# Optimization experiments

Hardware: AMD Instinct MI355X
Metric: run time of the kernel (lower is better)

## Reference

```python
import jax, jax.numpy as jnp
import numpy as np
import math

B, T, C, H, L, V = 4, 2048, 256, 4, 2, 1024
HS = C // H  # head size


def setup_inputs() -> dict:
    key = jax.random.key(0)
    ks = jax.random.split(key, 10)
    s = 0.02
    return {
        "tokens": jax.random.randint(ks[0], (B, T), 0, V),
        "wte": s * jax.random.normal(ks[1], (V + 1, C), dtype=jnp.float32),
        "ln1_g": jnp.ones((L, C), jnp.float32),
        "ln1_b": jnp.zeros((L, C), jnp.float32),
        "attn_w": s * jax.random.normal(ks[2], (L, 3 * C, C), dtype=jnp.float32),
        "attn_b": jnp.zeros((L, 3 * C), jnp.float32),
        "proj_w": s * jax.random.normal(ks[3], (L, C, C), dtype=jnp.float32),
        "proj_b": jnp.zeros((L, C), jnp.float32),
        "embk": s * jax.random.normal(ks[4], (L, T, HS), dtype=jnp.float32),
        "embv": s * jax.random.normal(ks[5], (L, T, HS), dtype=jnp.float32),
        "ln2_g": jnp.ones((L, C), jnp.float32),
        "ln2_b": jnp.zeros((L, C), jnp.float32),
        "fc_w": s * jax.random.normal(ks[6], (L, 4 * C, C), dtype=jnp.float32),
        "fc_b": jnp.zeros((L, 4 * C), jnp.float32),
        "mproj_w": s * jax.random.normal(ks[7], (L, C, 4 * C), dtype=jnp.float32),
        "mproj_b": jnp.zeros((L, C), jnp.float32),
        "lnf_g": jnp.ones((C,), jnp.float32),
        "lnf_b": jnp.zeros((C,), jnp.float32),
        "head_w": s * jax.random.normal(ks[8], (V, C), dtype=jnp.float32),
    }


def _ln(x, g, b):
    mu = x.mean(-1, keepdims=True)
    var = x.var(-1, keepdims=True)
    return (x - mu) / jnp.sqrt(var + 1e-5) * g + b


def _gelu(x):  # NewGELU (tanh approximation)
    return 0.5 * x * (1.0 + jnp.tanh(math.sqrt(2.0 / math.pi) * (x + 0.044715 * x ** 3)))


def reference(tokens, wte, ln1_g, ln1_b, attn_w, attn_b, proj_w, proj_b,
              embk, embv, ln2_g, ln2_b, fc_w, fc_b, mproj_w, mproj_b,
              lnf_g, lnf_b, head_w):
    x = wte[tokens]  # [B,T,C]; no absolute pos emb in this model
    idx = jnp.arange(T)
    rel = jnp.tril(idx[:, None] - idx[None, :])  # [T,T] nonneg offsets
    causal = idx[:, None] >= idx[None, :]
    scale = 1.0 / math.sqrt(HS)
    for l in range(L):
        h = _ln(x, ln1_g[l], ln1_b[l])
        qkv = h @ attn_w[l].T + attn_b[l]  # [B,T,3C]
        q, k, v = jnp.split(qkv, 3, axis=-1)
        q = q.reshape(B, T, H, HS).transpose(0, 2, 1, 3)  # [B,H,T,hs]
        k = k.reshape(B, T, H, HS).transpose(0, 2, 1, 3)
        v = v.reshape(B, T, H, HS).transpose(0, 2, 1, 3)
        rk = embk[l][rel]  # [T,T,hs]
        rv = embv[l][rel]  # [T,T,hs]
        att = jnp.einsum('bhtd,bhsd->bhts', q, k) * scale \
            + jnp.einsum('bhtd,tsd->bhts', q, rk)
        att = jnp.where(causal, att, -jnp.inf)
        att = jax.nn.softmax(att, axis=-1)
        y = jnp.einsum('bhts,bhsd->bhtd', att, v) \
            + jnp.einsum('bhts,tsd->bhtd', att, rv)
        y = y.transpose(0, 2, 1, 3).reshape(B, T, C)
        x = x + (y @ proj_w[l].T + proj_b[l])
        h2 = _ln(x, ln2_g[l], ln2_b[l])
        x = x + (_gelu(h2 @ fc_w[l].T + fc_b[l]) @ mproj_w[l].T + mproj_b[l])
    x = _ln(x, lnf_g, lnf_b)
    return x @ head_w.T  # [B,T,V] logits
```

## Files before the change

### kernel.cpp

```cpp
#include <hip/hip_runtime.h>
#include <hip/hip_bf16.h>
#include <math.h>

#define BB 4
#define TT 2048
#define CC 256
#define HH 4
#define LL 2
#define VV 1024
#define HS 64
#define EPAD 2176
#define LOG2E 1.4426950408889634f

typedef __attribute__((ext_vector_type(8))) __bf16 bf16x8;
typedef __attribute__((ext_vector_type(4))) float f32x4;

#define MFMA16(a, b, c) __builtin_amdgcn_mfma_f32_16x16x32_bf16((a), (b), (c), 0, 0, 0)

__device__ __forceinline__ ushort f2bf(float f) {
    __hip_bfloat16 h = __float2bfloat16(f);
    return *reinterpret_cast<ushort*>(&h);
}
__device__ __forceinline__ float bf2f(ushort u) {
    union { uint i; float f; } c; c.i = ((uint)u) << 16; return c.f;
}

__device__ __forceinline__ void gload16(const void* g, void* l) {
    __builtin_amdgcn_global_load_lds(
        (const __attribute__((address_space(1))) void*)g,
        (__attribute__((address_space(3))) void*)l, 16, 0, 0);
}

__device__ __forceinline__ float gelu_f(float v) {
    return 0.5f * v * (1.0f + tanhf(0.7978845608028654f * (v + 0.044715f * v * v * v)));
}

__global__ void embed_kernel(const int* __restrict__ tok,
                             const float* __restrict__ wte,
                             float* __restrict__ x) {
    int row = blockIdx.x;
    int tid = threadIdx.x;
    int tk = tok[row];
    x[(size_t)row * CC + tid] = wte[(size_t)tk * CC + tid];
}

__global__ void cvt5_kernel(const float* __restrict__ w0, const float* __restrict__ w1,
                            const float* __restrict__ w2, const float* __restrict__ w3,
                            const float* __restrict__ w4,
                            ushort* __restrict__ o0, ushort* __restrict__ o1,
                            ushort* __restrict__ o2, ushort* __restrict__ o3,
                            ushort* __restrict__ o4) {
    int i = blockIdx.x * 256 + threadIdx.x;
    const float* src; ushort* dst; int j;
    if (i < 98304)       { src = w0; dst = o0; j = i; }
    else if (i < 131072) { src = w1; dst = o1; j = i - 98304; }
    else if (i < 262144) { src = w2; dst = o2; j = i - 131072; }
    else if (i < 393216) { src = w3; dst = o3; j = i - 262144; }
    else                 { src = w4; dst = o4; j = i - 393216; }
    float4 v = ((const float4*)src)[j];
    ushort4 o;
    o.x = f2bf(v.x); o.y = f2bf(v.y); o.z = f2bf(v.z); o.w = f2bf(v.w);
    ((ushort4*)dst)[j] = o;
}

__global__ __launch_bounds__(256) void ln_kernel(const float* __restrict__ x,
                                                 const float* __restrict__ g,
                                                 const float* __restrict__ b,
                                                 ushort* __restrict__ out) {
    int row = blockIdx.x * 4 + (threadIdx.x >> 6);
    int lane = threadIdx.x & 63;
    float4 v = ((const float4*)(x + (size_t)row * CC))[lane];
    float s = v.x + v.y + v.z + v.w;
    float s2 = v.x * v.x + v.y * v.y + v.z * v.z + v.w * v.w;
    for (int m = 1; m < 64; m <<= 1) {
        s += __shfl_xor(s, m);
        s2 += __shfl_xor(s2, m);
    }
    float mean = s * (1.0f / CC);
    float var = s2 * (1.0f / CC) - mean * mean;
    float rs = rsqrtf(var + 1e-5f);
    float4 gg = ((const float4*)g)[lane];
    float4 bb = ((const float4*)b)[lane];
    ushort4 o;
    o.x = f2bf((v.x - mean) * rs * gg.x + bb.x);
    o.y = f2bf((v.y - mean) * rs * gg.y + bb.y);
    o.z = f2bf((v.z - mean) * rs * gg.z + bb.z);
    o.w = f2bf((v.w - mean) * rs * gg.w + bb.w);
    ((ushort4*)(out + (size_t)row * CC))[lane] = o;
}

template<int MODE>
__global__ __launch_bounds__(512) void bgemm256_kernel(
        const ushort* __restrict__ A, const ushort* __restrict__ W,
        const float* __restrict__ bias, float* __restrict__ out,
        ushort* __restrict__ outb, int N, int K,
        ushort* __restrict__ qb, ushort* __restrict__ kb,
        ushort* __restrict__ vtb) {
    constexpr int BUFSH = 16 * 512;
    __shared__ ushort lds[2 * BUFSH];
    int tid = threadIdx.x;
    int w = tid >> 6, lane = tid & 63;
    int lo = lane & 15, hi = lane >> 4;
    int row0 = blockIdx.y * 128;
    int col0 = blockIdx.x * 128;
    int wm = w >> 2, wn = w & 3;
    const ushort* Asrc = A + (size_t)row0 * K;
    const ushort* Wsrc = W + (size_t)col0 * K;

    auto STAGE = [&](int buf, int k0) {
        ushort* dst = &lds[buf * BUFSH];
        gload16(Asrc + (size_t)(w * 16 + lo) * K + k0 + hi * 8, dst + w * 512);
        gload16(Wsrc + (size_t)(w * 16 + lo) * K + k0 + hi * 8, dst + (8 + w) * 512);
    };

    f32x4 acc[4][2] = {};
    int NT = K >> 5;
    STAGE(0, 0);
    asm volatile("s_waitcnt vmcnt(0)" ::: "memory");
    __syncthreads();
    for (int t = 0; t < NT; ++t) {
        int buf = t & 1;
        if (t + 1 < NT) STAGE(buf ^ 1, (t + 1) << 5);
        bf16x8 a[4], b[2];
#pragma unroll
        for (int f = 0; f < 4; ++f)
            a[f] = *(const bf16x8*)&lds[buf * BUFSH + (wm * 4 + f) * 512 + lane * 8];
#pragma unroll
        for (int g = 0; g < 2; ++g)
            b[g] = *(const bf16x8*)&lds[buf * BUFSH + (8 + wn * 2 + g) * 512 + lane * 8];
        __builtin_amdgcn_s_setprio(1);
#pragma unroll
        for (int f = 0; f < 4; ++f)
#pragma unroll
            for (int g = 0; g < 2; ++g)
                acc[f][g] = MFMA16(a[f], b[g], acc[f][g]);
        __builtin_amdgcn_s_setprio(0);
        asm volatile("s_waitcnt vmcnt(0)" ::: "memory");
        __syncthreads();
    }
#pragma unroll
    for (int f = 0; f < 4; ++f) {
        int rr = row0 + wm * 64 + f * 16 + hi * 4;
#pragma unroll
        for (int g = 0; g < 2; ++g) {
            int cc = col0 + wn * 32 + g * 16 + lo;
            float bv = bias ? bias[cc] : 0.0f;
#pragma unroll
            for (int j = 0; j < 4; ++j) {
                int r = rr + j;
                float v = acc[f][g][j] + bv;
                if (MODE == 3) {
                    int t = r & 2047, bb2 = r >> 11;
                    int which = cc >> 8, hh = (cc >> 6) & 3, dd = cc & 63;
                    size_t bh = (size_t)(bb2 * 4 + hh);
                    if (which == 0)      qb[(bh * 2048 + t) * 64 + dd] = f2bf(v);
                    else if (which == 1) kb[(bh * 2048 + t) * 64 + dd] = f2bf(v * (0.125f * LOG2E));
                    else                 vtb[(bh * 64 + dd) * 2048 + t] = f2bf(v);
                } else if (MODE == 2) {
                    outb[(size_t)r * N + cc] = f2bf(gelu_f(v));
                } else {
                    out[(size_t)r * N + cc] = v;
                }
            }
        }
    }
}

__global__ __launch_bounds__(256) void bgemm64_kernel(
        const ushort* __restrict__ A, const ushort* __restrict__ W,
        const float* __restrict__ bias, float* __restrict__ out,
        int N, int K) {
    constexpr int ASUB = 8, TOT = 16, BUFSH = 128 * 64;
    __shared__ ushort lds[2 * BUFSH];
    int tid = threadIdx.x;
    int w = tid >> 6, lane = tid & 63;
    int lo = lane & 15, hi = lane >> 4;
    int row0 = blockIdx.y * 64;
    int col0 = blockIdx.x * 64;
    const ushort* Asrc = A + (size_t)row0 * K;
    const ushort* Wsrc = W + (size_t)col0 * K;

    auto STAGE = [&](int buf, int k0) {
        ushort* dst = &lds[buf * BUFSH];
        for (int s = w; s < TOT; s += 4) {
            const ushort* src;
            if (s < ASUB) {
                int rg = s >> 1, kh = s & 1;
                src = Asrc + (size_t)(rg * 16 + lo) * K + k0 + kh * 32 + hi * 8;
            } else {
                int s2 = s - ASUB;
                int cg = s2 >> 1, kh = s2 & 1;
                src = Wsrc + (size_t)(cg * 16 + lo) * K + k0 + kh * 32 + hi * 8;
            }
            gload16(src, dst + s * 512);
        }
    };

    f32x4 acc[4] = {};
    int NT = K >> 6;
    STAGE(0, 0);
    asm volatile("s_waitcnt vmcnt(0)" ::: "memory");
    __syncthreads();
    for (int t = 0; t < NT; ++t) {
        int buf = t & 1;
        if (t + 1 < NT) STAGE(buf ^ 1, (t + 1) << 6);
        bf16x8 a[2];
#pragma unroll
        for (int kh = 0; kh < 2; ++kh)
            a[kh] = *(const bf16x8*)&lds[buf * BUFSH + (w * 2 + kh) * 512 + lane * 8];
        __builtin_amdgcn_s_setprio(1);
#pragma unroll
        for (int g = 0; g < 4; ++g) {
#pragma unroll
            for (int kh = 0; kh < 2; ++kh) {
                bf16x8 b = *(const bf16x8*)&lds[buf * BUFSH + (ASUB + g * 2 + kh) * 512 + lane * 8];
                acc[g] = MFMA16(a[kh], b, acc[g]);
            }
        }
        __builtin_amdgcn_s_setprio(0);
        asm volatile("s_waitcnt vmcnt(0)" ::: "memory");
        __syncthreads();
    }
#pragma unroll
    for (int g = 0; g < 4; ++g) {
        int cc = col0 + g * 16 + lo;
        float bv = bias ? bias[cc] : 0.0f;
#pragma unroll
        for (int j = 0; j < 4; ++j) {
            int r = row0 + w * 16 + hi * 4 + j;
            out[(size_t)r * N + cc] += acc[g][j] + bv;
        }
    }
}

__global__ void emb_bf2_kernel(const float* __restrict__ ek,
                               const float* __restrict__ ev,
                               ushort* __restrict__ ekp,
                               ushort* __restrict__ evtp) {
    int i = blockIdx.x * 256 + threadIdx.x;
    int l = i / (EPAD * 64);
    int j = i - l * (EPAD * 64);
    int rp = j >> 6, d = j & 63;
    int o = rp - 64;
    bool in = (o >= 0 && o < TT);
    float kv = in ? ek[(size_t)l * TT * HS + (size_t)o * 64 + d] * LOG2E : 0.0f;
    float vv = in ? ev[(size_t)l * TT * HS + (size_t)o * 64 + d] : 0.0f;
    ekp[(size_t)l * EPAD * 64 + (size_t)rp * 64 + d] = f2bf(kv);
    evtp[(size_t)l * 64 * EPAD + (size_t)d * EPAD + rp] = f2bf(vv);
}

#define SBUF 57344
#define KOFF 0
#define VOFF 8192
#define EKOFF 16384
#define EVOFF 32768
#define WSCR (2 * SBUF)

__global__ __launch_bounds__(512, 2) void flash_kernel(
        const ushort* __restrict__ qb,
        const ushort* __restrict__ kb,
        const ushort* __restrict__ vtb,
        const ushort* __restrict__ ekp,
        const ushort* __restrict__ evtp,
        ushort* __restrict__ y) {
    extern __shared__ __align__(16) char dls[];

    int g = blockIdx.x;
    int lbid = ((g & 7) << 5) | (g >> 3);
    int bh = lbid >> 4;
    int pk = lbid & 15;
    int tid = threadIdx.x;
    int w = tid >> 6;
    int sub = w & 3;
    int h = w >> 2;
    int lane = tid & 63;
    int lo = lane & 15, hi = lane >> 4;
    int sw = (lo & 7) << 4;

    char* wbase = dls + WSCR + w * 6144;
    ushort (*Rl)[88]   = (ushort (*)[88])  wbase;
    ushort (*Pl)[72]   = (ushort (*)[72])  wbase;
    ushort (*Ppl)[104] = (ushort (*)[104])(wbase + 2816);

    {
        uint* pz = reinterpret_cast<uint*>(&Ppl[0][0]);
        for (int i = lane; i < 832; i += 64) pz[i] = 0;
    }

    const char* kB  = (const char*)(kb  + (size_t)bh * 2048 * 64);
    const char* vB  = (const char*)(vtb + (size_t)bh * 64 * 2048);
    const char* ekB = (const char*)ekp;
    const char* evB = (const char*)evtp;

    int t0A = (31 - pk) * 64, t0B = pk * 64;
    int NSA = 32 - pk;
    const int NC = 33;

    auto STAGE = [&](int buf, int ci) {
        int t0 = (ci < NSA) ? t0A : t0B;
        int s0 = ((ci < NSA) ? ci : ci - NSA) * 64;
        int band0 = t0 - s0;
        char* B = dls + buf * SBUF;
        int wb = (tid & 448) << 4;
        {
            int gb = tid * 16;
            int r = gb >> 7, c = gb & 127;
            gload16(kB + (size_t)(s0 + r) * 128 + (c ^ ((r & 7) << 4)), B + KOFF + wb);
        }
        {
            int gb = tid * 16;
            int r = gb >> 7, c = gb & 127;
            gload16(vB + (size_t)r * 4096 + (size_t)s0 * 2 + (c ^ ((r & 7) << 4)),
                    B + VOFF + wb);
        }
#pragma unroll
        for (int p = 0; p < 2; ++p) {
            int gb = p * 8192 + tid * 16;
            int r = gb >> 7, c = gb & 127;
            gload16(ekB + (size_t)(band0 + r) * 128 + (c ^ ((r & 7) << 4)),
                    B + EKOFF + p * 8192 + wb);
        }
#pragma unroll
        for (int p = 0; p < 3; ++p) {
            int gb = p * 8192 + tid * 16;
            int r = gb / 384, c = gb - r * 384;
            gload16(evB + (size_t)r * 4352 + (size_t)band0 * 2 + (c ^ ((r & 7) << 4)),
                    B + EVOFF + p * 8192 + wb);
        }
    };

    STAGE(0, 0);
    asm volatile("s_waitcnt vmcnt(0)" ::: "memory");
    __syncthreads();

    int b_ = bh >> 2, h_ = bh & 3;
    int buf = 0, ci = 0;
    int nb = h ? 0 : 2;
    int kcA = h ? 0 : 1, kcB = h ? 1 : 2;

    for (int tile = 0; tile < 2; ++tile) {
        int t0 = tile ? t0B : t0A;
        int NS = tile ? (pk + 1) : NSA;

        const ushort* qbase = qb + ((size_t)bh * 2048 + t0 + sub * 16) * 64;
        bf16x8 qf0 = *(const bf16x8*)(qbase + (size_t)lo * 64 + hi * 8);
        bf16x8 qf1 = *(const bf16x8*)(qbase + (size_t)lo * 64 + 32 + hi * 8);

        float rs[4] = {0.0f, 0.0f, 0.0f, 0.0f};
        f32x4 O[4] = {};

        for (int c = 0; c < NS; ++c, ++ci) {
            if (ci + 1 < NC) STAGE(buf ^ 1, ci + 1);
            const char* B = dls + buf * SBUF;
            bool diag = (c == NS - 1);

            f32x4 sacc[2] = {};
            __builtin_amdgcn_s_setprio(1);
#pragma unroll
            for (int ni = 0; ni < 2; ++ni) {
                int R = (2 * h + ni) * 16 + lo;
                bf16x8 b0 = *(const bf16x8*)(B + KOFF + R * 128 + ((hi * 16) ^ sw));
                bf16x8 b1 = *(const bf16x8*)(B + KOFF + R * 128 + ((64 + hi * 16) ^ sw));
                sacc[ni] = MFMA16(qf0, b0, sacc[ni]);
                sacc[ni] = MFMA16(qf1, b1, sacc[ni]);
            }
#pragma unroll
            for (int ni = 0; ni < 3; ++ni) {
                int n = nb + ni;
                int RL = (sub + n) * 16 + lo;
                f32x4 r = {};
                bf16x8 e0 = *(const bf16x8*)(B + EKOFF + RL * 128 + ((hi * 16) ^ sw));
                bf16x8 e1 = *(const bf16x8*)(B + EKOFF + RL * 128 + ((64 + hi * 16) ^ sw));
                r = MFMA16(qf0, e0, r);
                r = MFMA16(qf1, e1, r);
#pragma unroll
                for (int j = 0; j < 4; ++j) Rl[hi * 4 + j][n * 16 + lo] = f2bf(r[j]);
            }
            __builtin_amdgcn_s_setprio(0);
            float sv[2][4];
#pragma unroll
            for (int ni = 0; ni < 2; ++ni) {
                int sl = (2 * h + ni) * 16 + lo;
#pragma unroll
                for (int j = 0; j < 4; ++j) {
                    int r_ = hi * 4 + j;
                    sv[ni][j] = sacc[ni][j] + bf2f(Rl[r_][r_ - sl + 64]);
                }
            }
            asm volatile("" ::: "memory");
#pragma unroll
            for (int ni = 0; ni < 2; ++ni) {
                int sl = (2 * h + ni) * 16 + lo;
#pragma unroll
                for (int j = 0; j < 4; ++j) {
                    int r_ = hi * 4 + j;
                    float p = (!diag || sl <= sub * 16 + r_) ? exp2f(sv[ni][j]) : 0.0f;
                    rs[j] += p;
                    ushort pu = f2bf(p);
                    Pl[r_][sl] = pu;
                    Ppl[r_][r_ - sl + 64] = pu;
                }
            }
            asm volatile("" ::: "memory");

            __builtin_amdgcn_s_setprio(1);
            bf16x8 pa  = *(const bf16x8*)(&Pl[lo][h * 32 + hi * 8]);
            bf16x8 pb0 = *(const bf16x8*)(&Ppl[lo][kcA * 32 + hi * 8]);
            bf16x8 pb1 = *(const bf16x8*)(&Ppl[lo][kcB * 32 + hi * 8]);
#pragma unroll
            for (int n = 0; n < 4; ++n) {
                int R = n * 16 + lo;
                bf16x8 bv = *(const bf16x8*)(B + VOFF + R * 128 + ((h * 64 + hi * 16) ^ sw));
                O[n] = MFMA16(pa, bv, O[n]);
                bf16x8 e0 = *(const bf16x8*)(B + EVOFF + R * 384 +
                                             ((sub * 32 + kcA * 64 + hi * 16) ^ sw));
                O[n] = MFMA16(pb0, e0, O[n]);
                bf16x8 e1 = *(const bf16x8*)(B + EVOFF + R * 384 +
                                             ((sub * 32 + kcB * 64 + hi * 16) ^ sw));
                O[n] = MFMA16(pb1, e1, O[n]);
            }
            __builtin_amdgcn_s_setprio(0);
            asm volatile("" ::: "memory");

            asm volatile("s_waitcnt vmcnt(0)" ::: "memory");
            __syncthreads();
            buf ^= 1;
        }

#pragma unroll
        for (int msk = 1; msk < 16; msk <<= 1)
#pragma unroll
            for (int j = 0; j < 4; ++j) rs[j] += __shfl_xor(rs[j], msk);

        char* mscr = dls + (buf ^ 1) * SBUF + sub * 8192;
        if (h == 1) {
            float* Of = (float*)mscr;
#pragma unroll
            for (int n = 0; n < 4; ++n)
#pragma unroll
                for (int j = 0; j < 4; ++j)
                    Of[(hi * 4 + j) * 64 + n * 16 + lo] = O[n][j];
            if (lo == 0)
#pragma unroll
                for (int j = 0; j < 4; ++j)
                    ((float*)(mscr + 4096))[hi * 4 + j] = rs[j];
        }
        __syncthreads();
        if (h == 0) {
            float* Of = (float*)mscr;
            float inv[4];
#pragma unroll
            for (int j = 0; j < 4; ++j)
                inv[j] = 1.0f / (rs[j] + ((float*)(mscr + 4096))[hi * 4 + j]);
#pragma unroll
            for (int n = 0; n < 4; ++n)
#pragma unroll
                for (int j = 0; j < 4; ++j) {
                    int r = t0 + sub * 16 + hi * 4 + j;
                    float v = O[n][j] + Of[(hi * 4 + j) * 64 + n * 16 + lo];
                    y[((size_t)(b_ * 2048 + r)) * 256 + h_ * 64 + n * 16 + lo] =
                        f2bf(v * inv[j]);
                }
        }
        __syncthreads();
    }
}

extern "C" void kernel_launch(void* const* d_in, const int* in_sizes, int n_in,
                              void* d_out, int out_size, void* d_ws, size_t ws_size,
                              hipStream_t stream) {
    const int*   tokens  = (const int*)d_in[0];
    const float* wte     = (const float*)d_in[1];
    const float* ln1_g   = (const float*)d_in[2];
    const float* ln1_b   = (const float*)d_in[3];
    const float* attn_w  = (const float*)d_in[4];
    const float* attn_b  = (const float*)d_in[5];
    const float* proj_w  = (const float*)d_in[6];
    const float* proj_b  = (const float*)d_in[7];
    const float* embk    = (const float*)d_in[8];
    const float* embv    = (const float*)d_in[9];
    const float* ln2_g   = (const float*)d_in[10];
    const float* ln2_b   = (const float*)d_in[11];
    const float* fc_w    = (const float*)d_in[12];
    const float* fc_b    = (const float*)d_in[13];
    const float* mproj_w = (const float*)d_in[14];
    const float* mproj_b = (const float*)d_in[15];
    const float* lnf_g   = (const float*)d_in[16];
    const float* lnf_b   = (const float*)d_in[17];
    const float* head_w  = (const float*)d_in[18];
    float* out = (float*)d_out;

    const int M = BB * TT;
    char* wsb = (char*)d_ws;
    float*  x    = (float*)wsb;
    ushort* h    = (ushort*)(wsb + ((size_t)8 << 20));
    ushort* y    = (ushort*)(wsb + ((size_t)12 << 20));
    ushort* qb   = (ushort*)(wsb + ((size_t)16 << 20));
    ushort* kbf  = (ushort*)(wsb + ((size_t)20 << 20));
    ushort* vtb  = (ushort*)(wsb + ((size_t)24 << 20));
    ushort* ekp  = (ushort*)(wsb + ((size_t)28 << 20));
    ushort* evtp = ekp + (size_t)LL * EPAD * 64;
    ushort* attn_wb  = (ushort*)(wsb + ((size_t)30 << 20));
    ushort* proj_wb  = attn_wb + (size_t)LL * 3 * CC * CC;
    ushort* fc_wb    = proj_wb + (size_t)LL * CC * CC;
    ushort* mproj_wb = fc_wb + (size_t)LL * 4 * CC * CC;
    ushort* head_wb  = mproj_wb + (size_t)LL * CC * 4 * CC;
    ushort* fcb = (ushort*)d_out;

    dim3 blk(256);
    const int FLDS = WSCR + 8 * 6144;
    hipFuncSetAttribute(reinterpret_cast<const void*>(flash_kernel),
                        hipFuncAttributeMaxDynamicSharedMemorySize, FLDS);

    cvt5_kernel<<<dim3(1792), blk, 0, stream>>>(
        attn_w, proj_w, fc_w, mproj_w, head_w,
        attn_wb, proj_wb, fc_wb, mproj_wb, head_wb);
    emb_bf2_kernel<<<dim3(LL * EPAD * 64 / 256), blk, 0, stream>>>(
        embk, embv, ekp, evtp);
    embed_kernel<<<dim3(M), blk, 0, stream>>>(tokens, wte, x);

    for (int l = 0; l < LL; l++) {
        ln_kernel<<<dim3(M / 4), blk, 0, stream>>>(x, ln1_g + l * CC, ln1_b + l * CC, h);
        bgemm256_kernel<3><<<dim3(6, 64), dim3(512), 0, stream>>>(
            h, attn_wb + (size_t)l * 3 * CC * CC, attn_b + (size_t)l * 3 * CC,
            nullptr, nullptr, 3 * CC, CC, qb, kbf, vtb);
        flash_kernel<<<dim3(256), dim3(512), FLDS, stream>>>(
            qb, kbf, vtb, ekp + (size_t)l * EPAD * 64, evtp + (size_t)l * 64 * EPAD, y);
        bgemm64_kernel<<<dim3(4, 128), blk, 0, stream>>>(
            y, proj_wb + (size_t)l * CC * CC, proj_b + (size_t)l * CC,
            x, CC, CC);
        ln_kernel<<<dim3(M / 4), blk, 0, stream>>>(x, ln2_g + l * CC, ln2_b + l * CC, h);
        bgemm256_kernel<2><<<dim3(8, 64), dim3(512), 0, stream>>>(
            h, fc_wb + (size_t)l * 4 * CC * CC, fc_b + (size_t)l * 4 * CC,
            nullptr, fcb, 4 * CC, CC, nullptr, nullptr, nullptr);
        bgemm64_kernel<<<dim3(4, 128), blk, 0, stream>>>(
            fcb, mproj_wb + (size_t)l * CC * 4 * CC, mproj_b + (size_t)l * CC,
            x, CC, 4 * CC);
    }

    ln_kernel<<<dim3(M / 4), blk, 0, stream>>>(x, lnf_g, lnf_b, h);
    bgemm256_kernel<0><<<dim3(8, 64), dim3(512), 0, stream>>>(
        h, head_wb, nullptr, out, nullptr, VV, CC, nullptr, nullptr, nullptr);
}
```

Measured before the change: 331.0 us.

## Fuse residual-add and LayerNorm into projection GEMMs; merge prep and embed kernels

The two residual projection GEMMs (attn proj and MLP proj) now compute a full 256-wide row strip per block of 32 rows. Each block adds bias and residual, then reduces row statistics through shuffles and LDS to emit the next LayerNorm's bf16 output directly. This removes the separate ln kernels. The embedding lookup is fused with the first LayerNorm, and the weight and relative-embedding conversion kernels are merged into one launch. The cost is fewer, larger blocks: 256 blocks, each re-streaming the whole weight matrix, and the extra LDS may lower occupancy.

```diff
diff --git a/kernel.cpp b/kernel.cpp
--- a/kernel.cpp
+++ b/kernel.cpp
@@ -35,41 +35,49 @@
     return 0.5f * v * (1.0f + tanhf(0.7978845608028654f * (v + 0.044715f * v * v * v)));
 }
 
-__global__ void embed_kernel(const int* __restrict__ tok,
-                             const float* __restrict__ wte,
-                             float* __restrict__ x) {
-    int row = blockIdx.x;
-    int tid = threadIdx.x;
-    int tk = tok[row];
-    x[(size_t)row * CC + tid] = wte[(size_t)tk * CC + tid];
-}
-
-__global__ void cvt5_kernel(const float* __restrict__ w0, const float* __restrict__ w1,
+__global__ void prep_kernel(const float* __restrict__ w0, const float* __restrict__ w1,
                             const float* __restrict__ w2, const float* __restrict__ w3,
                             const float* __restrict__ w4,
                             ushort* __restrict__ o0, ushort* __restrict__ o1,
                             ushort* __restrict__ o2, ushort* __restrict__ o3,
-                            ushort* __restrict__ o4) {
-    int i = blockIdx.x * 256 + threadIdx.x;
-    const float* src; ushort* dst; int j;
-    if (i < 98304)       { src = w0; dst = o0; j = i; }
-    else if (i < 131072) { src = w1; dst = o1; j = i - 98304; }
-    else if (i < 262144) { src = w2; dst = o2; j = i - 131072; }
-    else if (i < 393216) { src = w3; dst = o3; j = i - 262144; }
-    else                 { src = w4; dst = o4; j = i - 393216; }
-    float4 v = ((const float4*)src)[j];
-    ushort4 o;
-    o.x = f2bf(v.x); o.y = f2bf(v.y); o.z = f2bf(v.z); o.w = f2bf(v.w);
-    ((ushort4*)dst)[j] = o;
-}
-
-__global__ __launch_bounds__(256) void ln_kernel(const float* __restrict__ x,
-                                                 const float* __restrict__ g,
-                                                 const float* __restrict__ b,
-                                                 ushort* __restrict__ out) {
+                            ushort* __restrict__ o4,
+                            const float* __restrict__ ek, const float* __restrict__ ev,
+                            ushort* __restrict__ ekp, ushort* __restrict__ evtp) {
+    int bi = blockIdx.x;
+    if (bi < 1792) {
+        int i = bi * 256 + threadIdx.x;
+        const float* src; ushort* dst; int j;
+        if (i < 98304)       { src = w0; dst = o0; j = i; }
+        else if (i < 131072) { src = w1; dst = o1; j = i - 98304; }
+        else if (i < 262144) { src = w2; dst = o2; j = i - 131072; }
+        else if (i < 393216) { src = w3; dst = o3; j = i - 262144; }
+        else                 { src = w4; dst = o4; j = i - 393216; }
+        float4 v = ((const float4*)src)[j];
+        ushort4 o;
+        o.x = f2bf(v.x); o.y = f2bf(v.y); o.z = f2bf(v.z); o.w = f2bf(v.w);
+        ((ushort4*)dst)[j] = o;
+    } else {
+        int i = (bi - 1792) * 256 + threadIdx.x;
+        int l = i / (EPAD * 64);
+        int j = i - l * (EPAD * 64);
+        int rp = j >> 6, d = j & 63;
+        int o = rp - 64;
+        bool in = (o >= 0 && o < TT);
+        float kv = in ? ek[(size_t)l * TT * HS + (size_t)o * 64 + d] * LOG2E : 0.0f;
+        float vv = in ? ev[(size_t)l * TT * HS + (size_t)o * 64 + d] : 0.0f;
+        ekp[(size_t)l * EPAD * 64 + (size_t)rp * 64 + d] = f2bf(kv);
+        evtp[(size_t)l * 64 * EPAD + (size_t)d * EPAD + rp] = f2bf(vv);
+    }
+}
+
+__global__ __launch_bounds__(256) void embed_ln_kernel(
+        const int* __restrict__ tok, const float* __restrict__ wte,
+        const float* __restrict__ g, const float* __restrict__ b,
+        float* __restrict__ x, ushort* __restrict__ h) {
     int row = blockIdx.x * 4 + (threadIdx.x >> 6);
     int lane = threadIdx.x & 63;
-    float4 v = ((const float4*)(x + (size_t)row * CC))[lane];
+    int tk = tok[row];
+    float4 v = ((const float4*)(wte + (size_t)tk * CC))[lane];
     float s = v.x + v.y + v.z + v.w;
     float s2 = v.x * v.x + v.y * v.y + v.z * v.z + v.w * v.w;
     for (int m = 1; m < 64; m <<= 1) {
@@ -86,7 +94,8 @@
     o.y = f2bf((v.y - mean) * rs * gg.y + bb.y);
     o.z = f2bf((v.z - mean) * rs * gg.z + bb.z);
     o.w = f2bf((v.w - mean) * rs * gg.w + bb.w);
-    ((ushort4*)(out + (size_t)row * CC))[lane] = o;
+    ((float4*)(x + (size_t)row * CC))[lane] = v;
+    ((ushort4*)(h + (size_t)row * CC))[lane] = o;
 }
 
 template<int MODE>
@@ -166,87 +175,112 @@
     }
 }
 
-__global__ __launch_bounds__(256) void bgemm64_kernel(
+template<int NSTEP>
+__global__ __launch_bounds__(512) void bgemmln_kernel(
         const ushort* __restrict__ A, const ushort* __restrict__ W,
-        const float* __restrict__ bias, float* __restrict__ out,
-        int N, int K) {
-    constexpr int ASUB = 8, TOT = 16, BUFSH = 128 * 64;
-    __shared__ ushort lds[2 * BUFSH];
+        const float* __restrict__ bias, float* __restrict__ x,
+        const float* __restrict__ lng, const float* __restrict__ lnb,
+        ushort* __restrict__ hout) {
+    extern __shared__ ushort plds[];
+    constexpr int K = NSTEP * 64;
+    constexpr int BUFSH = 36 * 512;
     int tid = threadIdx.x;
     int w = tid >> 6, lane = tid & 63;
     int lo = lane & 15, hi = lane >> 4;
-    int row0 = blockIdx.y * 64;
-    int col0 = blockIdx.x * 64;
+    int row0 = blockIdx.x * 32;
+    int wm = w >> 2, wn = w & 3;
     const ushort* Asrc = A + (size_t)row0 * K;
-    const ushort* Wsrc = W + (size_t)col0 * K;
 
     auto STAGE = [&](int buf, int k0) {
-        ushort* dst = &lds[buf * BUFSH];
-        for (int s = w; s < TOT; s += 4) {
+        ushort* dst = &plds[buf * BUFSH];
+        for (int s = w; s < 36; s += 8) {
             const ushort* src;
-            if (s < ASUB) {
+            if (s < 4) {
                 int rg = s >> 1, kh = s & 1;
                 src = Asrc + (size_t)(rg * 16 + lo) * K + k0 + kh * 32 + hi * 8;
             } else {
-                int s2 = s - ASUB;
-                int cg = s2 >> 1, kh = s2 & 1;
-                src = Wsrc + (size_t)(cg * 16 + lo) * K + k0 + kh * 32 + hi * 8;
+                int sb = s - 4, cg = sb >> 1, kh = sb & 1;
+                src = W + (size_t)(cg * 16 + lo) * K + k0 + kh * 32 + hi * 8;
             }
             gload16(src, dst + s * 512);
         }
     };
 
     f32x4 acc[4] = {};
-    int NT = K >> 6;
     STAGE(0, 0);
     asm volatile("s_waitcnt vmcnt(0)" ::: "memory");
     __syncthreads();
-    for (int t = 0; t < NT; ++t) {
+    for (int t = 0; t < NSTEP; ++t) {
         int buf = t & 1;
-        if (t + 1 < NT) STAGE(buf ^ 1, (t + 1) << 6);
+        if (t + 1 < NSTEP) STAGE(buf ^ 1, (t + 1) << 6);
         bf16x8 a[2];
 #pragma unroll
         for (int kh = 0; kh < 2; ++kh)
-            a[kh] = *(const bf16x8*)&lds[buf * BUFSH + (w * 2 + kh) * 512 + lane * 8];
+            a[kh] = *(const bf16x8*)&plds[buf * BUFSH + (wm * 2 + kh) * 512 + lane * 8];
         __builtin_amdgcn_s_setprio(1);
 #pragma unroll
-        for (int g = 0; g < 4; ++g) {
+        for (int g2 = 0; g2 < 4; ++g2) {
 #pragma unroll
             for (int kh = 0; kh < 2; ++kh) {
-                bf16x8 b = *(const bf16x8*)&lds[buf * BUFSH + (ASUB + g * 2 + kh) * 512 + lane * 8];
-                acc[g] = MFMA16(a[kh], b, acc[g]);
+                bf16x8 b = *(const bf16x8*)&plds[buf * BUFSH + 2048 +
+                                                 ((wn * 4 + g2) * 2 + kh) * 512 + lane * 8];
+                acc[g2] = MFMA16(a[kh], b, acc[g2]);
             }
         }
         __builtin_amdgcn_s_setprio(0);
         asm volatile("s_waitcnt vmcnt(0)" ::: "memory");
         __syncthreads();
     }
-#pragma unroll
-    for (int g = 0; g < 4; ++g) {
-        int cc = col0 + g * 16 + lo;
-        float bv = bias ? bias[cc] : 0.0f;
+
+    float* part = (float*)&plds[2 * BUFSH];
+    float v[4][4];
+    float s1[4] = {0, 0, 0, 0}, s2[4] = {0, 0, 0, 0};
+#pragma unroll
+    for (int g2 = 0; g2 < 4; ++g2) {
+        int cc = wn * 64 + g2 * 16 + lo;
+        float bv = bias[cc];
 #pragma unroll
         for (int j = 0; j < 4; ++j) {
-            int r = row0 + w * 16 + hi * 4 + j;
-            out[(size_t)r * N + cc] += acc[g][j] + bv;
-        }
-    }
-}
-
-__global__ void emb_bf2_kernel(const float* __restrict__ ek,
-                               const float* __restrict__ ev,
-                               ushort* __restrict__ ekp,
-                               ushort* __restrict__ evtp) {
-    int i = blockIdx.x * 256 + threadIdx.x;
-    int l = i / (EPAD * 64);
-    int j = i - l * (EPAD * 64);
-    int rp = j >> 6, d = j & 63;
-    int o = rp - 64;
-    bool in = (o >= 0 && o < TT);
-    float kv = in ? ek[(size_t)l * TT * HS + (size_t)o * 64 + d] * LOG2E : 0.0f;
-    float vv = in ? ev[(size_t)l * TT * HS + (size_t)o * 64 + d] : 0.0f;
-    ekp[(size_t)l * EPAD * 64 + (size_t)rp * 64 + d] = f2bf(kv);
-    evtp[(size_t)l * 64 * EPAD + (size_t)d * EPAD + rp] = f2bf(vv);
+            int r = row0 + wm * 16 + hi * 4 + j;
+            float tv = acc[g2][j] + bv + x[(size_t)r * CC + cc];
+            v[g2][j] = tv;
+            s1[j] += tv;
+            s2[j] += tv * tv;
+        }
+    }
+#pragma unroll
+    for (int msk = 1; msk < 16; msk <<= 1)
+#pragma unroll
+        for (int j = 0; j < 4; ++j) {
+            s1[j] += __shfl_xor(s1[j], msk);
+            s2[j] += __shfl_xor(s2[j], msk);
+        }
+    if (lo == 0) {
+#pragma unroll
+        for (int j = 0; j < 4; ++j) {
+            int rr = wm * 16 + hi * 4 + j;
+            part[rr * 4 + wn] = s1[j];
+            part[128 + rr * 4 + wn] = s2[j];
+        }
+    }
+    __syncthreads();
+#pragma unroll
+    for (int j = 0; j < 4; ++j) {
+        int rr = wm * 16 + hi * 4 + j;
+        int r = row0 + rr;
+        float4 p1 = *(float4*)&part[rr * 4];
+        float4 p2 = *(float4*)&part[128 + rr * 4];
+        float mean = (p1.x + p1.y + p1.z + p1.w) * (1.0f / CC);
+        float var = (p2.x + p2.y + p2.z + p2.w) * (1.0f / CC) - mean * mean;
+        float rsd = rsqrtf(var + 1e-5f);
+#pragma unroll
+        for (int g2 = 0; g2 < 4; ++g2) {
+            int cc = wn * 64 + g2 * 16 + lo;
+            x[(size_t)r * CC + cc] = v[g2][j];
+            hout[(size_t)r * CC + cc] =
+                f2bf((v[g2][j] - mean) * rsd * lng[cc] + lnb[cc]);
+        }
+    }
 }
 
 #define SBUF 57344
@@ -509,36 +543,41 @@
 
     dim3 blk(256);
     const int FLDS = WSCR + 8 * 6144;
+    const int PLDS = 2 * 36864 + 1024;
     hipFuncSetAttribute(reinterpret_cast<const void*>(flash_kernel),
                         hipFuncAttributeMaxDynamicSharedMemorySize, FLDS);
-
-    cvt5_kernel<<<dim3(1792), blk, 0, stream>>>(
+    hipFuncSetAttribute(reinterpret_cast<const void*>(bgemmln_kernel<4>),
+                        hipFuncAttributeMaxDynamicSharedMemorySize, PLDS);
+    hipFuncSetAttribute(reinterpret_cast<const void*>(bgemmln_kernel<16>),
+                        hipFuncAttributeMaxDynamicSharedMemorySize, PLDS);
+
+    prep_kernel<<<dim3(2880), blk, 0, stream>>>(
         attn_w, proj_w, fc_w, mproj_w, head_w,
-        attn_wb, proj_wb, fc_wb, mproj_wb, head_wb);
-    emb_bf2_kernel<<<dim3(LL * EPAD * 64 / 256), blk, 0, stream>>>(
+        attn_wb, proj_wb, fc_wb, mproj_wb, head_wb,
         embk, embv, ekp, evtp);
-    embed_kernel<<<dim3(M), blk, 0, stream>>>(tokens, wte, x);
+
+    embed_ln_kernel<<<dim3(M / 4), blk, 0, stream>>>(
+        tokens, wte, ln1_g, ln1_b, x, h);
 
     for (int l = 0; l < LL; l++) {
-        ln_kernel<<<dim3(M / 4), blk, 0, stream>>>(x, ln1_g + l * CC, ln1_b + l * CC, h);
         bgemm256_kernel<3><<<dim3(6, 64), dim3(512), 0, stream>>>(
             h, attn_wb + (size_t)l * 3 * CC * CC, attn_b + (size_t)l * 3 * CC,
             nullptr, nullptr, 3 * CC, CC, qb, kbf, vtb);
         flash_kernel<<<dim3(256), dim3(512), FLDS, stream>>>(
             qb, kbf, vtb, ekp + (size_t)l * EPAD * 64, evtp + (size_t)l * 64 * EPAD, y);
-        bgemm64_kernel<<<dim3(4, 128), blk, 0, stream>>>(
+        bgemmln_kernel<4><<<dim3(256), dim3(512), PLDS, stream>>>(
             y, proj_wb + (size_t)l * CC * CC, proj_b + (size_t)l * CC,
-            x, CC, CC);
-        ln_kernel<<<dim3(M / 4), blk, 0, stream>>>(x, ln2_g + l * CC, ln2_b + l * CC, h);
+            x, ln2_g + l * CC, ln2_b + l * CC, h);
         bgemm256_kernel<2><<<dim3(8, 64), dim3(512), 0, stream>>>(
             h, fc_wb + (size_t)l * 4 * CC * CC, fc_b + (size_t)l * 4 * CC,
             nullptr, fcb, 4 * CC, CC, nullptr, nullptr, nullptr);
-        bgemm64_kernel<<<dim3(4, 128), blk, 0, stream>>>(
+        const float* ng = (l == 0) ? (ln1_g + CC) : lnf_g;
+        const float* nb = (l == 0) ? (ln1_b + CC) : lnf_b;
+        bgemmln_kernel<16><<<dim3(256), dim3(512), PLDS, stream>>>(
             fcb, mproj_wb + (size_t)l * CC * 4 * CC, mproj_b + (size_t)l * CC,
-            x, CC, 4 * CC);
-    }
-
-    ln_kernel<<<dim3(M / 4), blk, 0, stream>>>(x, lnf_g, lnf_b, h);
+            x, ng, nb, h);
+    }
+
     bgemm256_kernel<0><<<dim3(8, 64), dim3(512), 0, stream>>>(
         h, head_wb, nullptr, out, nullptr, VV, CC, nullptr, nullptr, nullptr);
 }
```

Measured after the change: 324.2 us. -2.1%, faster.
